# Kernel optimization log

Measured on AMD Instinct MI355X. Metric: run time of the kernel, lower is better.

The kernel has to match this reference:

```python
import jax, jax.numpy as jnp
import numpy as np

EPSILON = float(np.finfo(np.float32).tiny)
K = 64      # top-k edges to keep
TAU = 0.1   # gumbel-softmax temperature


def setup_inputs() -> dict:
    key = jax.random.key(0)
    k1, k2 = jax.random.split(key)
    B, N, E = 64, 256, 4
    scores = jax.random.normal(k1, (B, N, N, E), dtype=jnp.float32)
    # Gumbel(0,1) noise matching flat_scores shape [B*E, N*N]
    gumbel = jax.random.gumbel(k2, (B * E, N * N), dtype=jnp.float32)
    return {"scores": scores, "gumbel": gumbel}


def reference(scores, gumbel):
    B, N, _, E = scores.shape
    local_k = min(K, N * N)
    # [B, N, N, E] -> [B, E, N, N] -> [B*E, N*N]
    flat = scores.transpose(0, 3, 1, 2).reshape(B * E, N * N) + gumbel
    khot = jnp.zeros_like(flat)
    onehot = jnp.zeros_like(flat)

    def step(carry, _):
        flat, khot, onehot = carry
        khot_mask = jnp.maximum(1.0 - onehot, EPSILON)
        flat = flat + jnp.log(khot_mask)
        onehot = jax.nn.softmax(flat / TAU, axis=1)
        return (flat, khot + onehot, onehot), None

    (flat, khot, onehot), _ = jax.lax.scan(
        step, (flat, khot, onehot), None, length=local_k)

    # hard straight-through top-k
    _, ind = jax.lax.top_k(khot, local_k)                 # [B*E, local_k]
    rows = jnp.arange(khot.shape[0])[:, None]
    khot_hard = jnp.zeros_like(khot).at[rows, ind].set(1.0)
    res = khot_hard - jax.lax.stop_gradient(khot) + khot

    # [B*E, N*N] -> [B, E, N, N] -> [B, N, N, E]
    new_mask = res.reshape(B, E, N, N).transpose(0, 2, 3, 1)
    return new_mask
```

## Files before the change

kernel.cpp:

```cpp
#include <hip/hip_runtime.h>
#include <cfloat>

#define NROW   256
#define RLEN   65536
#define TPB    1024
#define VPT    64
#define REGS   8
#define MAXC   (TPB*REGS)
#define NITER  64
#define KSEL   64
#define THETA_OFF 8.0f
#define TCAP   256
#define LN_TGT 7.6246f
#define GATE  (-18.03f)

__global__ void __launch_bounds__(TPB, 4)
GumbelSampler_2482491097709_kernel(const float* __restrict__ scores,
                                   const float* __restrict__ gumbel,
                                   float* __restrict__ out)
{
    __shared__ float s_P[2][16];
    __shared__ float s_EA[16];
    __shared__ float s_EB[16];
    __shared__ int   s_IC[16];
    __shared__ float s_Lse[NITER];
    __shared__ int   s_cnt;
    __shared__ int   s_selB;
    __shared__ int   s_selR;
    __shared__ int   s_tcnt;
    __shared__ int   s_tie[TCAP];
    __shared__ int   s_hist[4096];
    __shared__ int   cand_idx[MAXC];
    __shared__ float cand_kv[MAXC];

    const int tid  = threadIdx.x;
    const int lane = tid & 63;
    const int wid  = tid >> 6;

    const int q    = blockIdx.x;
    const int xcd  = q & 7;
    const int slot = q >> 3;
    const int b    = xcd * 8 + (slot & 7);
    const int e    = slot >> 3;
    const int r    = b * 4 + e;

    const float* __restrict__ sr = scores + (size_t)b * (RLEN * 4) + e;
    const float* __restrict__ gr = gumbel + (size_t)r * RLEN;

    float v[VPT];
    float lm = -FLT_MAX;
#pragma unroll
    for (int s = 0; s < VPT; ++s) {
        int p = tid + TPB * s;
        float x = sr[(size_t)p * 4] + gr[p];
        v[s] = x;
        lm = fmaxf(lm, x);
    }
#pragma unroll
    for (int s = 0; s < VPT; ++s) asm volatile("" : "+v"(v[s]));

#pragma unroll
    for (int o = 32; o; o >>= 1) lm = fmaxf(lm, __shfl_xor(lm, o));
    if (lane == 0) s_P[0][wid] = lm;
    __syncthreads();
    float M0 = s_P[0][lane & 15];
#pragma unroll
    for (int o = 8; o; o >>= 1) M0 = fmaxf(M0, __shfl_xor(M0, o));
    const float C = M0 * 10.0f;

    float theta = M0 - THETA_OFF;
    for (int probe = 0; probe < 12; ++probe) {
        int lc = 0;
#pragma unroll
        for (int s = 0; s < VPT; ++s) lc += (v[s] >= theta) ? 1 : 0;
#pragma unroll
        for (int o = 32; o; o >>= 1) lc += __shfl_xor(lc, o);
        if (lane == 0) s_IC[wid] = lc;
        __syncthreads();
        int cc = s_IC[lane & 15];
#pragma unroll
        for (int o = 8; o; o >>= 1) cc += __shfl_xor(cc, o);
        __syncthreads();
        if (cc > MAXC - 64)      theta += __logf((float)cc) - LN_TGT;
        else if (cc < KSEL)      theta -= LN_TGT - __logf((float)(cc < 1 ? 1 : cc));
        else break;
    }

    if (tid == 0) s_cnt = 0;
    __syncthreads();
    {
        float mu = -FLT_MAX, u = 0.f;
#pragma unroll
        for (int s = 0; s < VPT; ++s) {
            float val = v[s];
            bool pr = (val >= theta);
            unsigned long long m = __ballot(pr);
            if (pr) {
                int lead = __ffsll(m) - 1;
                int base = 0;
                if (lane == lead) base = atomicAdd(&s_cnt, (int)__popcll(m));
                base = __shfl(base, lead);
                int sl = base + (int)__popcll(m & ((1ull << lane) - 1ull));
                if (sl < MAXC) { cand_idx[sl] = tid + TPB * s; cand_kv[sl] = val; }
            } else {
                mu = fmaxf(mu, val);
                float yv = fmaf(val, 10.f, -C);
                if (yv > -87.f) u += __expf(yv);
            }
        }
#pragma unroll
        for (int o = 32; o; o >>= 1) {
            mu = fmaxf(mu, __shfl_xor(mu, o));
            u += __shfl_xor(u, o);
        }
        if (lane == 0) { s_EA[wid] = mu; s_EB[wid] = u; }
    }
    __syncthreads();
    int cnt = s_cnt;
    float Mu = s_EA[lane & 15], U = s_EB[lane & 15];
#pragma unroll
    for (int o = 8; o; o >>= 1) {
        Mu = fmaxf(Mu, __shfl_xor(Mu, o));
        U += __shfl_xor(U, o);
    }

    float rcur[REGS];
#pragma unroll
    for (int j = 0; j < REGS; ++j) {
        int sl = tid + TPB * j;
        if (sl < cnt) {
            rcur[j] = cand_kv[sl];
            cand_kv[sl] = 0.f;
        } else rcur[j] = 0.f;
    }

    bool  noexp = false;
    float anc = C;
    for (int t = 0; t < NITER; ++t) {
        const int pb = t & 1;
        float ls = 0.f;
        if (t == 0) {
#pragma unroll
            for (int j = 0; j < REGS; ++j)
                if (tid + TPB * j < cnt)
                    ls += __expf(fmaf(rcur[j], 10.f, -anc));
        } else {
#pragma unroll
            for (int j = 0; j < REGS; ++j) {
                int sl = tid + TPB * j;
                if (sl < cnt) {
                    float cur = rcur[j];
                    float y = fmaf(cur, 10.f, -anc);
                    float e_ = __expf(y);
                    if (y > GATE) {
                        cand_kv[sl] += e_;
                        cur += __logf(fmaxf(1.f - e_, FLT_MIN));
                        rcur[j] = cur;
                        e_ = __expf(fmaf(cur, 10.f, -anc));
                    }
                    ls += e_;
                }
            }
        }
#pragma unroll
        for (int o = 32; o; o >>= 1) ls += __shfl_xor(ls, o);
        if (lane == 0) s_P[pb][wid] = ls;
        __syncthreads();
        float S = s_P[pb][lane & 15];
#pragma unroll
        for (int o = 8; o; o >>= 1) S += __shfl_xor(S, o);
        if (U > 0.f) S += __expf(C - anc + __logf(U));
        float Lse = anc + __logf(S);
        if (tid == 0) s_Lse[t] = Lse;

        if (!noexp && t < NITER - 1 && 10.f * Mu > Lse - 20.f) {
            float thOld = theta;
            float thN   = (Lse - 26.f) * 0.1f;
            int   oldc  = cnt;
            float mu2 = -FLT_MAX, u2 = 0.f;
#pragma unroll 4
            for (int s = 0; s < VPT; ++s) {
                int p = tid + TPB * s;
                float val = sr[(size_t)p * 4] + gr[p];
                if (val < thOld) {
                    if (val >= thN) {
                        int sl = atomicAdd(&s_cnt, 1);
                        if (sl < MAXC) {
                            cand_idx[sl] = p;
                            cand_kv[sl]  = val;
                        }
                    } else {
                        mu2 = fmaxf(mu2, val);
                        float yv = fmaf(val, 10.f, -C);
                        if (yv > -87.f) u2 += __expf(yv);
                    }
                }
            }
#pragma unroll
            for (int o = 32; o; o >>= 1) {
                mu2 = fmaxf(mu2, __shfl_xor(mu2, o));
                u2 += __shfl_xor(u2, o);
            }
            if (lane == 0) { s_EA[wid] = mu2; s_EB[wid] = u2; }
            __syncthreads();
            int newc = s_cnt;
            if (newc > MAXC) {
                if (tid == 0) s_cnt = oldc;
                noexp = true;
            } else {
                float m2 = s_EA[lane & 15], uu = s_EB[lane & 15];
#pragma unroll
                for (int o = 8; o; o >>= 1) {
                    m2 = fmaxf(m2, __shfl_xor(m2, o));
                    uu += __shfl_xor(uu, o);
                }
                Mu = m2; U = uu; theta = thN;
#pragma unroll
                for (int j = 0; j < REGS; ++j) {
                    int sl = tid + TPB * j;
                    if (sl >= oldc && sl < newc) {
                        float vv = cand_kv[sl];
                        rcur[j] = vv;
                        float kb = 0.f;
                        for (int tt = 0; tt < t; ++tt)
                            kb += __expf(fmaf(vv, 10.f, -s_Lse[tt]));
                        cand_kv[sl] = kb;
                    }
                }
                cnt = newc;
            }
        }
        anc = Lse;
    }
#pragma unroll
    for (int j = 0; j < REGS; ++j) {
        int sl = tid + TPB * j;
        if (sl < cnt) {
            float y = fmaf(rcur[j], 10.f, -anc);
            if (y > GATE) cand_kv[sl] += __expf(y);
        }
    }
    __syncthreads();

    unsigned prefix = 0;
    int Rrem = KSEL;
    for (int pass = 0; pass < 3; ++pass) {
        const int nbins = (pass == 2) ? 1024 : 2048;
        for (int i = tid; i < nbins; i += TPB) s_hist[i] = 0;
        __syncthreads();
#pragma unroll
        for (int j = 0; j < REGS; ++j) {
            int sl = tid + TPB * j;
            if (sl < cnt) {
                unsigned key = __float_as_uint(cand_kv[sl]);
                if (key != 0u) {
                    bool m; int bin;
                    if (pass == 0)      { m = true;                     bin = key >> 21; }
                    else if (pass == 1) { m = (key >> 21) == prefix;    bin = (key >> 10) & 2047; }
                    else                { m = (key >> 10) == prefix;    bin = key & 1023; }
                    if (m) atomicAdd(&s_hist[bin], 1);
                }
            }
        }
        __syncthreads();
        if (wid == 0) {
            int Rl = Rrem, found = -1;
            const int nch = nbins >> 6;
            const int c0 = (pass == 0) ? 23 : 0;
            for (int c = c0; c < nch && found < 0; ++c) {
                int bin = nbins - 1 - (c * 64 + lane);
                int h = s_hist[bin];
                int cum = h;
#pragma unroll
                for (int s2 = 1; s2 < 64; s2 <<= 1) {
                    int vv = __shfl_up(cum, s2);
                    if (lane >= s2) cum += vv;
                }
                unsigned long long mb = __ballot(cum >= Rl);
                if (mb) {
                    int fl = __ffsll(mb) - 1;
                    int cumex = __shfl(cum, fl) - __shfl(h, fl);
                    found = nbins - 1 - (c * 64 + fl);
                    Rl -= cumex;
                } else {
                    Rl -= __shfl(cum, 63);
                }
            }
            if (lane == 0) { s_selB = found; s_selR = Rl; }
        }
        __syncthreads();
        prefix = (prefix << ((pass == 2) ? 10 : 11)) | (unsigned)s_selB;
        Rrem = s_selR;
    }
    const unsigned Kstar = prefix;
    const int need = Rrem;

    if (tid == 0) s_tcnt = 0;
    __syncthreads();
#pragma unroll
    for (int j = 0; j < REGS; ++j) {
        int sl = tid + TPB * j;
        if (sl < cnt) {
            float kh = cand_kv[sl];
            unsigned key = __float_as_uint(kh);
            if (key > Kstar) {
                int p = cand_idx[sl];
                out[((size_t)b * RLEN + (size_t)p) * 4 + e] = (1.f - kh) + kh;
            } else if (key == Kstar) {
                int tp = atomicAdd(&s_tcnt, 1);
                if (tp < TCAP) s_tie[tp] = cand_idx[sl];
            }
        }
    }
    __syncthreads();
    if (wid == 0) {
        int T = s_tcnt < TCAP ? s_tcnt : TCAP;
        float kv = __uint_as_float(Kstar);
        float ov = (1.f - kv) + kv;
        for (int rdone = 0; rdone < need; ++rdone) {
            int bi = 0x7fffffff, bp = -1;
            for (int i = lane; i < T; i += 64) {
                int vv = s_tie[i];
                if (vv < bi) { bi = vv; bp = i; }
            }
#pragma unroll
            for (int s2 = 32; s2; s2 >>= 1) {
                int oi = __shfl_xor(bi, s2);
                int op = __shfl_xor(bp, s2);
                if (oi < bi) { bi = oi; bp = op; }
            }
            if (lane == 0 && bi != 0x7fffffff) {
                out[((size_t)b * RLEN + (size_t)bi) * 4 + e] = ov;
                s_tie[bp] = 0x7fffffff;
            }
        }
    }
}

extern "C" void kernel_launch(void* const* d_in, const int* in_sizes, int n_in,
                              void* d_out, int out_size, void* d_ws, size_t ws_size,
                              hipStream_t stream) {
    const float* scores = (const float*)d_in[0];
    const float* gumbel = (const float*)d_in[1];
    float* out = (float*)d_out;

    hipMemsetAsync(d_out, 0, (size_t)out_size * sizeof(float), stream);
    GumbelSampler_2482491097709_kernel<<<NROW, TPB, 0, stream>>>(scores, gumbel, out);
}
```

Baseline: 343.7 us.

## Reformulate iterative softmax in linear double-precision weight domain

Replaces the log-domain per-iteration update (exp/log per candidate per step) with multiplicative weights w = exp(10(x-M0)) kept in double precision. The log(1-onehot)*10 update becomes w *= (1-o)^10 via repeated squaring, and the softmax output is w/S. Late-admitted candidates get their accumulated khot in closed form as w*sum(1/S), which removes the inner loop over past Lse values. This trades transcendental calls for FP64 multiplies, which are relatively fast on MI355X, but it doubles register footprint for w and kh.

```diff
diff --git a/kernel.cpp b/kernel.cpp
--- a/kernel.cpp
+++ b/kernel.cpp
@@ -1,5 +1,6 @@
 #include <hip/hip_runtime.h>
 #include <cfloat>
+#include <math.h>
 
 #define NROW   256
 #define RLEN   65536
@@ -12,18 +13,17 @@
 #define THETA_OFF 8.0f
 #define TCAP   256
 #define LN_TGT 7.6246f
-#define GATE  (-18.03f)
+#define WGATE_D 1.4787e-8
 
 __global__ void __launch_bounds__(TPB, 4)
 GumbelSampler_2482491097709_kernel(const float* __restrict__ scores,
                                    const float* __restrict__ gumbel,
                                    float* __restrict__ out)
 {
-    __shared__ float s_P[2][16];
+    __shared__ double s_Pd[2][16];
     __shared__ float s_EA[16];
     __shared__ float s_EB[16];
     __shared__ int   s_IC[16];
-    __shared__ float s_Lse[NITER];
     __shared__ int   s_cnt;
     __shared__ int   s_selB;
     __shared__ int   s_selR;
@@ -61,12 +61,13 @@
 
 #pragma unroll
     for (int o = 32; o; o >>= 1) lm = fmaxf(lm, __shfl_xor(lm, o));
-    if (lane == 0) s_P[0][wid] = lm;
-    __syncthreads();
-    float M0 = s_P[0][lane & 15];
+    if (lane == 0) s_EA[wid] = lm;
+    __syncthreads();
+    float M0 = s_EA[lane & 15];
 #pragma unroll
     for (int o = 8; o; o >>= 1) M0 = fmaxf(M0, __shfl_xor(M0, o));
-    const float C = M0 * 10.0f;
+    const float  C  = M0 * 10.0f;
+    const double M0d = (double)M0;
 
     float theta = M0 - THETA_OFF;
     for (int probe = 0; probe < 12; ++probe) {
@@ -117,65 +118,63 @@
     }
     __syncthreads();
     int cnt = s_cnt;
-    float Mu = s_EA[lane & 15], U = s_EB[lane & 15];
+    float Mu = s_EA[lane & 15], Uf = s_EB[lane & 15];
 #pragma unroll
     for (int o = 8; o; o >>= 1) {
         Mu = fmaxf(Mu, __shfl_xor(Mu, o));
-        U += __shfl_xor(U, o);
-    }
-
-    float rcur[REGS];
+        Uf += __shfl_xor(Uf, o);
+    }
+    double Ud = (double)Uf;
+
+    double w[REGS], kh[REGS];
 #pragma unroll
     for (int j = 0; j < REGS; ++j) {
         int sl = tid + TPB * j;
-        if (sl < cnt) {
-            rcur[j] = cand_kv[sl];
-            cand_kv[sl] = 0.f;
-        } else rcur[j] = 0.f;
-    }
-
-    bool  noexp = false;
-    float anc = C;
+        if (sl < cnt) w[j] = exp(10.0 * ((double)cand_kv[sl] - M0d));
+        else          w[j] = 0.0;
+        kh[j] = 0.0;
+    }
+
+    bool   noexp = false;
+    double rcpS = 0.0, wT = 1e300;
+    double Rsum = 0.0;
+    double Ktrig = exp(fma(10.0, (double)Mu, -10.0 * M0d + 20.0));
     for (int t = 0; t < NITER; ++t) {
         const int pb = t & 1;
-        float ls = 0.f;
-        if (t == 0) {
-#pragma unroll
-            for (int j = 0; j < REGS; ++j)
-                if (tid + TPB * j < cnt)
-                    ls += __expf(fmaf(rcur[j], 10.f, -anc));
-        } else {
-#pragma unroll
-            for (int j = 0; j < REGS; ++j) {
-                int sl = tid + TPB * j;
-                if (sl < cnt) {
-                    float cur = rcur[j];
-                    float y = fmaf(cur, 10.f, -anc);
-                    float e_ = __expf(y);
-                    if (y > GATE) {
-                        cand_kv[sl] += e_;
-                        cur += __logf(fmaxf(1.f - e_, FLT_MIN));
-                        rcur[j] = cur;
-                        e_ = __expf(fmaf(cur, 10.f, -anc));
-                    }
-                    ls += e_;
-                }
+        double ls = 0.0;
+#pragma unroll
+        for (int j = 0; j < REGS; ++j) {
+            int sl = tid + TPB * j;
+            if (sl < cnt) {
+                double wj = w[j];
+                double o  = wj * rcpS;
+                kh[j] += o;
+                if (wj > wT) {
+                    double m  = 1.0 - o;
+                    double m2 = m * m;
+                    double m4 = m2 * m2;
+                    double m8 = m4 * m4;
+                    wj *= m8 * m2;
+                    w[j] = wj;
+                }
+                ls += wj;
             }
         }
 #pragma unroll
         for (int o = 32; o; o >>= 1) ls += __shfl_xor(ls, o);
-        if (lane == 0) s_P[pb][wid] = ls;
-        __syncthreads();
-        float S = s_P[pb][lane & 15];
+        if (lane == 0) s_Pd[pb][wid] = ls;
+        __syncthreads();
+        double S = s_Pd[pb][lane & 15];
 #pragma unroll
         for (int o = 8; o; o >>= 1) S += __shfl_xor(S, o);
-        if (U > 0.f) S += __expf(C - anc + __logf(U));
-        float Lse = anc + __logf(S);
-        if (tid == 0) s_Lse[t] = Lse;
-
-        if (!noexp && t < NITER - 1 && 10.f * Mu > Lse - 20.f) {
+        S += Ud;
+        rcpS = 1.0 / S;
+        wT   = S * WGATE_D;
+
+        if (!noexp && t < NITER - 1 && S < Ktrig) {
+            double Lse  = fma(10.0, M0d, log(S));
             float thOld = theta;
-            float thN   = (Lse - 26.f) * 0.1f;
+            float thN   = (float)((Lse - 26.0) * 0.1);
             int   oldc  = cnt;
             float mu2 = -FLT_MAX, u2 = 0.f;
 #pragma unroll 4
@@ -208,36 +207,34 @@
                 if (tid == 0) s_cnt = oldc;
                 noexp = true;
             } else {
-                float m2 = s_EA[lane & 15], uu = s_EB[lane & 15];
+                float m2_ = s_EA[lane & 15], uu = s_EB[lane & 15];
 #pragma unroll
                 for (int o = 8; o; o >>= 1) {
-                    m2 = fmaxf(m2, __shfl_xor(m2, o));
+                    m2_ = fmaxf(m2_, __shfl_xor(m2_, o));
                     uu += __shfl_xor(uu, o);
                 }
-                Mu = m2; U = uu; theta = thN;
+                Mu = m2_; Ud = (double)uu; theta = thN;
+                Ktrig = exp(fma(10.0, (double)Mu, -10.0 * M0d + 20.0));
 #pragma unroll
                 for (int j = 0; j < REGS; ++j) {
                     int sl = tid + TPB * j;
                     if (sl >= oldc && sl < newc) {
-                        float vv = cand_kv[sl];
-                        rcur[j] = vv;
-                        float kb = 0.f;
-                        for (int tt = 0; tt < t; ++tt)
-                            kb += __expf(fmaf(vv, 10.f, -s_Lse[tt]));
-                        cand_kv[sl] = kb;
+                        double wn = exp(10.0 * ((double)cand_kv[sl] - M0d));
+                        w[j]  = wn;
+                        kh[j] = wn * Rsum;
                     }
                 }
                 cnt = newc;
             }
         }
-        anc = Lse;
+        Rsum += rcpS;
     }
 #pragma unroll
     for (int j = 0; j < REGS; ++j) {
         int sl = tid + TPB * j;
         if (sl < cnt) {
-            float y = fmaf(rcur[j], 10.f, -anc);
-            if (y > GATE) cand_kv[sl] += __expf(y);
+            kh[j] += w[j] * rcpS;
+            cand_kv[sl] = (float)kh[j];
         }
     }
     __syncthreads();
@@ -301,11 +298,11 @@
     for (int j = 0; j < REGS; ++j) {
         int sl = tid + TPB * j;
         if (sl < cnt) {
-            float kh = cand_kv[sl];
-            unsigned key = __float_as_uint(kh);
+            float khf = cand_kv[sl];
+            unsigned key = __float_as_uint(khf);
             if (key > Kstar) {
                 int p = cand_idx[sl];
-                out[((size_t)b * RLEN + (size_t)p) * 4 + e] = (1.f - kh) + kh;
+                out[((size_t)b * RLEN + (size_t)p) * 4 + e] = (1.f - khf) + khf;
             } else if (key == Kstar) {
                 int tp = atomicAdd(&s_tcnt, 1);
                 if (tp < TCAP) s_tie[tp] = cand_idx[sl];
```

Measured after the change: 360.0 us. 1.05x slower.
